# Kernel optimization log

Measured on AMD Instinct MI355X. Metric: run time of the kernel, lower is better.

## Reference

```python
import jax, jax.numpy as jnp
import numpy as np

K = 8            # hard-coded knn k
NS = 0.2         # LeakyReLU negative slope
EPS = 1e-6
LN_EPS = 1e-5
H = 6            # num_heads


def vn_lin(W, x):
    # VNLinear: linear over vector-channel dim (axis 1). x: (B, Cin, 3, ...)
    return jnp.einsum('oc,bc...->bo...', W, x)


def vn_leaky(x, W, U):
    # VNLinearLeakyReLU (no BN): feature map p, direction map d
    p = vn_lin(W, x)
    d = vn_lin(U, x)
    dot = jnp.sum(p * d, axis=2, keepdims=True)
    dsq = jnp.sum(d * d, axis=2, keepdims=True)
    neg = p - (dot / (dsq + EPS)) * d
    return NS * p + (1.0 - NS) * jnp.where(dot >= 0, p, neg)


def vn_layernorm(x, g, b):
    # LayerNorm on per-channel vector norms, rescale directions. x: (B,C,3,N)
    n = jnp.sqrt(jnp.sum(x * x, axis=2) + EPS)            # (B,C,N)
    mu = jnp.mean(n, axis=1, keepdims=True)
    var = jnp.var(n, axis=1, keepdims=True)
    nhat = (n - mu) / jnp.sqrt(var + LN_EPS)
    nnew = g[None, :, None] * nhat + b[None, :, None]
    return x * (nnew / n)[:, :, None, :]


def vn_attention(vn_x, Wq, Wk, Wv, Wo):
    # vn_x: (B, C, 3, N); VNLinear(C, 3C) projections, multi-head SDPA over N
    B, C, _, N = vn_x.shape
    def heads(W):
        t = vn_lin(W, vn_x)                               # (B, 3C, 3, N)
        t = t.reshape(B, H, 3 * C // H, 3, N)
        return t.transpose(0, 1, 4, 2, 3).reshape(B, H, N, -1)  # (B,H,N,9C/H)
    q, k, v = heads(Wq), heads(Wk), heads(Wv)
    scale = (3 * C // H) ** -0.5                          # head_dim = dim//H = 64
    attn = jax.nn.softmax(jnp.einsum('bhqd,bhkd->bhqk', q, k) * scale, axis=-1)
    o = jnp.einsum('bhqk,bhkd->bhqd', attn, v)            # (B,H,N,9C/H)
    o = o.transpose(0, 2, 1, 3).reshape(B, N, 3 * C, 3).transpose(0, 2, 3, 1)
    return vn_lin(Wo, o)                                  # (B, C, 3, N)


def vn_get_graph_feature(x, knn_index):
    # x: (B, C, 3, N); knn_index: flat (B*K*N,) into (B*N) rows
    B, C, _, N = x.shape
    xp = x.transpose(0, 3, 1, 2).reshape(B * N, C * 3)
    feat = xp[knn_index].reshape(B, K, N, C, 3)
    xc = x.transpose(0, 3, 1, 2).reshape(B, 1, N, C, 3)
    f = jnp.concatenate([feat - xc, jnp.broadcast_to(xc, (B, K, N, C, 3))], axis=3)
    return f.transpose(0, 3, 4, 2, 1)                     # (B, 2C, 3, N, K)


def setup_inputs() -> dict:
    key = jax.random.key(0)
    ks = jax.random.split(key, 20)
    B, N, C = 4, 2048, 128
    def w(k, o, i):
        return jax.random.normal(k, (o, i), jnp.float32) * (i ** -0.5)
    return {
        'x': jax.random.normal(ks[0], (B, N, 3 * C), jnp.float32),
        'knn_index': jax.random.randint(ks[1], (B * K * N,), 0, B * N),
        'g1': jnp.ones((C,), jnp.float32), 'b1': jnp.zeros((C,), jnp.float32),
        'g2': jnp.ones((C,), jnp.float32), 'b2': jnp.zeros((C,), jnp.float32),
        'Wq': w(ks[2], 3 * C, C), 'Wk': w(ks[3], 3 * C, C), 'Wv': w(ks[4], 3 * C, C),
        'Wo': w(ks[5], C, 3 * C),
        'W1': w(ks[6], C, 2 * C), 'U1': w(ks[7], C, 2 * C),   # conv1: 256->128
        'W2': w(ks[8], C, 2 * C),                               # conv2: 256->128
        'W3': w(ks[9], 2 * C, C), 'U3': w(ks[10], 2 * C, C),   # conv3: 128->256
        'W4': w(ks[11], C, 2 * C), 'U4': w(ks[12], C, 2 * C),  # conv4: 256->128
    }


def reference(x, knn_index, g1, b1, g2, b2, Wq, Wk, Wv, Wo, W1, U1, W2, W3, U3, W4, U4):
    B, N, D = x.shape
    C = D // 3
    vn_x = x.transpose(0, 2, 1).reshape(B, C, 3, N)
    norm_x = vn_layernorm(vn_x, g1, b1)
    x_1 = vn_attention(norm_x, Wq, Wk, Wv, Wo)            # (B,C,3,N)
    knn_f = vn_get_graph_feature(norm_x, knn_index)       # (B,2C,3,N,K)
    knn_f = vn_leaky(knn_f, W1, U1)                       # (B,C,3,N,K)
    knn_f = jnp.mean(knn_f, axis=-1)                      # mean_pool over k
    x_1 = jnp.concatenate([x_1, knn_f], axis=1)           # (B,2C,3,N)
    x_1 = vn_lin(W2, x_1)                                 # (B,C,3,N)
    vn_x = vn_x + x_1
    nx2 = vn_layernorm(vn_x, g2, b2)
    h = vn_leaky(nx2, W3, U3)                             # (B,2C,3,N)
    h = vn_leaky(h, W4, U4)                               # (B,C,3,N)
    vn_x = vn_x + h
    return vn_x.reshape(B, D, N).transpose(0, 2, 1)       # (B,N,384)
```

## Files before the change

kernel.cpp:

```cpp
#include <hip/hip_runtime.h>
#include <math.h>

#define NFIX 2048
#define HH 6
#define KNN 8
#define NSLOPE 0.2f
#define EPSF 1e-6f
#define LNEPSF 1e-5f
#define QSCALE 0.18033688011112042f
#define NSPLIT 2

typedef unsigned short ushort_t;
typedef unsigned int uint_t;
typedef __attribute__((ext_vector_type(8))) short bf16x8;
typedef __attribute__((ext_vector_type(4))) short bf16x4;
typedef __attribute__((ext_vector_type(8))) _Float16 f16x8;
typedef __attribute__((ext_vector_type(4))) _Float16 f16x4;
typedef __attribute__((ext_vector_type(16))) float f32x16;
typedef __attribute__((ext_vector_type(4))) float f32x4;

__device__ __forceinline__ ushort_t f2bf(float f) {
  union { float f; unsigned u; } v; v.f = f;
  unsigned r = v.u + 0x7fff + ((v.u >> 16) & 1);
  return (ushort_t)(r >> 16);
}
__device__ __forceinline__ float bf2f(ushort_t u) {
  union { uint_t u; float f; } v; v.u = ((uint_t)u) << 16; return v.f;
}
__device__ __forceinline__ uint_t pack2(float a, float b) {
  return (uint_t)f2bf(a) | ((uint_t)f2bf(b) << 16);
}
__device__ __forceinline__ ushort_t f2h_bits(float a) {
  union { _Float16 h; ushort_t s; } cv; cv.h = (_Float16)a; return cv.s;
}
__device__ __forceinline__ uint_t packh2(float a, float b) {
  union { _Float16 h; ushort_t s; } ha, hb;
  ha.h = (_Float16)a; hb.h = (_Float16)b;
  return (uint_t)ha.s | ((uint_t)hb.s << 16);
}

__device__ __forceinline__ void vnleaky3(const float* p, const float* dv, float* out) {
  float dot = p[0]*dv[0] + p[1]*dv[1] + p[2]*dv[2];
  float dsq = dv[0]*dv[0] + dv[1]*dv[1] + dv[2]*dv[2] + EPSF;
  float f = dot / dsq;
#pragma unroll
  for (int d = 0; d < 3; ++d) {
    float neg = p[d] - f * dv[d];
    out[d] = NSLOPE * p[d] + (1.f - NSLOPE) * ((dot >= 0.f) ? p[d] : neg);
  }
}

__global__ __launch_bounds__(256) void prep_ln1(
    const float* __restrict__ Wq, const float* __restrict__ Wk,
    const float* __restrict__ Wv, const float* __restrict__ Wo,
    const float* __restrict__ W1, const float* __restrict__ U1,
    const float* __restrict__ W2, const float* __restrict__ W3,
    const float* __restrict__ U3, const float* __restrict__ W4,
    const float* __restrict__ U4,
    ushort_t* __restrict__ Wall, _Float16* __restrict__ Af16,
    _Float16* __restrict__ W3h, _Float16* __restrict__ U3h,
    _Float16* __restrict__ W4h, _Float16* __restrict__ U4h,
    const float* __restrict__ xin, ushort_t* __restrict__ xbp,
    float* __restrict__ xdi, const float* __restrict__ g1,
    const float* __restrict__ b1) {
  __shared__ float red[8];
  int bi = blockIdx.x;
  if (bi >= 1600) {
    int t = threadIdx.x;
    int half = t >> 7, c = t & 127;
    int bn = (bi - 1600) * 2 + half;
    const float* row = xin + (size_t)bn * 384;
    float x0 = row[c*3+0], x1 = row[c*3+1], x2 = row[c*3+2];
    float nv = sqrtf(x0*x0 + x1*x1 + x2*x2 + EPSF);
    float s1 = nv, s2 = nv*nv;
#pragma unroll
    for (int off = 32; off >= 1; off >>= 1) {
      s1 += __shfl_down(s1, off);
      s2 += __shfl_down(s2, off);
    }
    int lane = t & 63, w = t >> 6;
    if (lane == 0) { red[w*2] = s1; red[w*2+1] = s2; }
    __syncthreads();
    int rb4 = (w >> 1) * 4;
    float tot1 = red[rb4] + red[rb4+2], tot2 = red[rb4+1] + red[rb4+3];
    float mu  = tot1 * (1.f/128.f);
    float var = tot2 * (1.f/128.f) - mu*mu;
    float rsig = rsqrtf(var + LNEPSF);
    float nnew = g1[c] * ((nv - mu) * rsig) + b1[c];
    float sc = nnew / nv;
    size_t rb = (size_t)bn * 384;
    xbp[rb + c]       = f2bf(x0*sc);
    xbp[rb + 128 + c] = f2bf(x1*sc);
    xbp[rb + 256 + c] = f2bf(x2*sc);
    xdi[rb + c]       = x0;
    xdi[rb + 128 + c] = x1;
    xdi[rb + 256 + c] = x2;
    return;
  }
  int idx = bi * 256 + threadIdx.x;
  if (idx < 212992) {
    int m = idx >> 7, c = idx & 127;
    float val;
    if (m < 384)       val = Wq[m*128 + c] * QSCALE;
    else if (m < 768)  val = Wk[(m-384)*128 + c];
    else if (m < 1152) val = Wv[(m-768)*128 + c];
    else {
      int j = m - 1152;
      if (j < 128)      val = W1[j*256 + c];
      else if (j < 256) val = U1[(j-128)*256 + c];
      else if (j < 384) { int o = j-256; val = W1[o*256 + 128 + c] - W1[o*256 + c]; }
      else              { int o = j-384; val = U1[o*256 + 128 + c] - U1[o*256 + c]; }
    }
    Wall[idx] = f2bf(val); return;
  }
  idx -= 212992;
  if (idx < 49152) {
    int c = idx / 384, j = idx % 384;
    float s = 0.f;
    for (int cp = 0; cp < 128; ++cp) s += W2[c*256 + cp] * Wo[cp*384 + j];
    Af16[(size_t)c*512 + j] = (_Float16)s; return;
  }
  idx -= 49152;
  if (idx < 16384) {
    int c2 = idx / 128, c = idx % 128;
    Af16[(size_t)c*512 + 384 + c2] = (_Float16)W2[c*256 + 128 + c2]; return;
  }
  idx -= 16384;
  if (idx < 32768) { W3h[idx] = (_Float16)W3[idx]; return; }
  idx -= 32768;
  if (idx < 32768) { U3h[idx] = (_Float16)U3[idx]; return; }
  idx -= 32768;
  if (idx < 32768) { W4h[idx] = (_Float16)W4[idx]; return; }
  idx -= 32768;
  if (idx < 32768) { U4h[idx] = (_Float16)U4[idx]; return; }
}

#define XT_PITCH 132
#define WT_PITCH 132
#define TR_PITCH 36
__global__ __launch_bounds__(256, 2) void qkv_conv1_mfma(
    const ushort_t* __restrict__ xb, const ushort_t* __restrict__ Wall,
    ushort_t* __restrict__ q, ushort_t* __restrict__ k, ushort_t* __restrict__ v,
    _Float16* __restrict__ YZh, _Float16* __restrict__ NBh) {
  __shared__ ushort_t xs[128*XT_PITCH];
  __shared__ ushort_t wt[2][32*WT_PITCH];
  __shared__ float tr[4][32*TR_PITCH];
  int nb = blockIdx.x % 192;
  int mq = blockIdx.x / 192;
  int n0 = nb * 128;
  int t = threadIdx.x;
  int w = t >> 6, lane = t & 63, ql = lane & 31, hl = lane >> 5;
  for (int idx = t; idx < 2048; idx += 256) {
    int n = idx >> 4, c16 = idx & 15;
    bf16x8 gv = *(const bf16x8*)&xb[(size_t)(n0 + n)*128 + c16*8];
    ushort_t* dst = &xs[n*XT_PITCH + c16*8];
    *(bf16x4*)dst = __builtin_shufflevector(gv, gv, 0, 1, 2, 3);
    *(bf16x4*)(dst+4) = __builtin_shufflevector(gv, gv, 4, 5, 6, 7);
  }
#pragma unroll
  for (int i = 0; i < 2; ++i) {
    int idx = i*256 + t;
    int mm = idx >> 4, c16 = idx & 15;
    bf16x8 gv = *(const bf16x8*)&Wall[(size_t)(mq*416 + mm)*128 + c16*8];
    ushort_t* dst = &wt[0][mm*WT_PITCH + c16*8];
    *(bf16x4*)dst = __builtin_shufflevector(gv, gv, 0, 1, 2, 3);
    *(bf16x4*)(dst+4) = __builtin_shufflevector(gv, gv, 4, 5, 6, 7);
  }
  __syncthreads();
  bf16x8 xf[8];
  {
    const ushort_t* xr = &xs[(w*32 + ql)*XT_PITCH + hl*8];
#pragma unroll
    for (int cs = 0; cs < 8; ++cs) {
      bf16x4 lo = *(const bf16x4*)(xr + cs*16);
      bf16x4 hi = *(const bf16x4*)(xr + cs*16 + 4);
      xf[cs] = __builtin_shufflevector(lo, hi, 0, 1, 2, 3, 4, 5, 6, 7);
    }
  }
  int ng = n0 + w*32 + ql;
  int pt = ng / 3;
  int d  = ng - 3*pt;
  float* trw = tr[w];
  int mm0 = t >> 4, c160 = t & 15;
  int mm1 = (t + 256) >> 4, c161 = t & 15;
  for (int mt = 0; mt < 13; ++mt) {
    int m0 = mq*416 + mt*32;
    int cur = mt & 1;
    bf16x8 wpre0, wpre1;
    if (mt < 12) {
      int m0n = m0 + 32;
      wpre0 = *(const bf16x8*)&Wall[(size_t)(m0n + mm0)*128 + c160*8];
      wpre1 = *(const bf16x8*)&Wall[(size_t)(m0n + mm1)*128 + c161*8];
    }
    f32x16 acc;
#pragma unroll
    for (int r = 0; r < 16; ++r) acc[r] = 0.f;
    const ushort_t* wr = &wt[cur][ql*WT_PITCH + hl*8];
#pragma unroll
    for (int cs = 0; cs < 8; ++cs) {
      bf16x4 lo = *(const bf16x4*)(wr + cs*16);
      bf16x4 hi = *(const bf16x4*)(wr + cs*16 + 4);
      bf16x8 af = __builtin_shufflevector(lo, hi, 0, 1, 2, 3, 4, 5, 6, 7);
      acc = __builtin_amdgcn_mfma_f32_32x32x16_bf16(af, xf[cs], acc, 0, 0, 0);
    }
#pragma unroll
    for (int r = 0; r < 16; ++r) {
      int mrow = (r&3) + 8*(r>>2) + 4*hl;
      trw[ql*TR_PITCH + mrow] = acc[r];
    }
    asm volatile("s_waitcnt lgkmcnt(0)" ::: "memory");
    float4 c0 = *(float4*)&trw[ql*TR_PITCH + hl*16 + 0];
    float4 c1 = *(float4*)&trw[ql*TR_PITCH + hl*16 + 4];
    float4 c2 = *(float4*)&trw[ql*TR_PITCH + hl*16 + 8];
    float4 c3 = *(float4*)&trw[ql*TR_PITCH + hl*16 + 12];
    asm volatile("s_waitcnt lgkmcnt(0)" ::: "memory");
    int mg = m0 + hl*16;
    if (m0 < 1152) {
      uint4 s0, s1;
      s0.x = pack2(c0.x, c0.y); s0.y = pack2(c0.z, c0.w);
      s0.z = pack2(c1.x, c1.y); s0.w = pack2(c1.z, c1.w);
      s1.x = pack2(c2.x, c2.y); s1.y = pack2(c2.z, c2.w);
      s1.z = pack2(c3.x, c3.y); s1.w = pack2(c3.z, c3.w);
      ushort_t* dst;
      if (m0 < 384)       dst = q + (size_t)pt*1152 + d*384 + mg;
      else if (m0 < 768)  dst = k + (size_t)pt*1152 + d*384 + (mg - 384);
      else                dst = v + (size_t)pt*1152 + d*384 + (mg - 768);
      *(uint4*)dst = s0;
      *(uint4*)(dst + 8) = s1;
    } else {
      int mat = mg - 1152;
      int sub = mat >> 7, o = mat & 127;
      _Float16* basep = (sub < 2) ? YZh : NBh;
      _Float16* dst = basep + (size_t)pt*768 + d*256 + (sub & 1)*128 + o;
      uint4 s0, s1;
      s0.x = packh2(c0.x, c0.y); s0.y = packh2(c0.z, c0.w);
      s0.z = packh2(c1.x, c1.y); s0.w = packh2(c1.z, c1.w);
      s1.x = packh2(c2.x, c2.y); s1.y = packh2(c2.z, c2.w);
      s1.z = packh2(c3.x, c3.y); s1.w = packh2(c3.z, c3.w);
      *(uint4*)dst = s0;
      *(uint4*)(dst + 8) = s1;
    }
    if (mt < 12) {
      int nxt = cur ^ 1;
      ushort_t* d0 = &wt[nxt][mm0*WT_PITCH + c160*8];
      *(bf16x4*)d0 = __builtin_shufflevector(wpre0, wpre0, 0, 1, 2, 3);
      *(bf16x4*)(d0+4) = __builtin_shufflevector(wpre0, wpre0, 4, 5, 6, 7);
      ushort_t* d1 = &wt[nxt][mm1*WT_PITCH + c161*8];
      *(bf16x4*)d1 = __builtin_shufflevector(wpre1, wpre1, 0, 1, 2, 3);
      *(bf16x4*)(d1+4) = __builtin_shufflevector(wpre1, wpre1, 4, 5, 6, 7);
    }
    __syncthreads();
  }
}

#define VT_LP 196
__global__ __launch_bounds__(256) void post_vtrans(const ushort_t* __restrict__ v,
    ushort_t* __restrict__ vT, const _Float16* __restrict__ YZh,
    const _Float16* __restrict__ NBh, const int* __restrict__ knn_index,
    _Float16* __restrict__ kmf16) {
  __shared__ ushort_t tl[64*VT_LP];
  __shared__ int sidx[8][KNN];
  int blk = blockIdx.x;
  int t = threadIdx.x;
  if (blk < 768) {
    int bh = blk / 32, ptile = blk % 32;
    int b = bh / HH, h = bh % HH;
    int pt0 = ptile * 64;
#pragma unroll
    for (int i = 0; i < 6; ++i) {
      int u = i*256 + t;
      int p = u / 24, seg = u % 24;
      int d = seg >> 3, c8 = seg & 7;
      bf16x8 gv = *(const bf16x8*)&v[(size_t)(b*NFIX + pt0 + p)*1152 + d*384 + h*64 + c8*8];
      ushort_t* dst = &tl[p*VT_LP + d*64 + c8*8];
      *(bf16x4*)dst = __builtin_shufflevector(gv, gv, 0, 1, 2, 3);
      *(bf16x4*)(dst+4) = __builtin_shufflevector(gv, gv, 4, 5, 6, 7);
    }
    __syncthreads();
#pragma unroll
    for (int i = 0; i < 6; ++i) {
      int u = i*256 + t;
      int ch = u >> 3, pc = u & 7;
      int ol = ch / 3, dd = ch - 3*ol;
      int cloc = dd*64 + ol;
      ushort_t hv[8];
#pragma unroll
      for (int e = 0; e < 8; ++e)
        hv[e] = tl[(pc*8 + e)*VT_LP + cloc];
      uint4 o4;
      o4.x = (uint_t)hv[0] | ((uint_t)hv[1] << 16);
      o4.y = (uint_t)hv[2] | ((uint_t)hv[3] << 16);
      o4.z = (uint_t)hv[4] | ((uint_t)hv[5] << 16);
      o4.w = (uint_t)hv[6] | ((uint_t)hv[7] << 16);
      *(uint4*)&vT[((size_t)bh*192 + ch)*2048 + pt0 + pc*8] = o4;
    }
    return;
  }
  int bnb = (blk - 768) * 8;
  int half = t >> 7, c = t & 127;
  if (t < 64) {
    int pi = t >> 3, kk = t & 7;
    int bn = bnb + pi;
    int b = bn / NFIX, n = bn % NFIX;
    sidx[pi][kk] = knn_index[(b*KNN + kk)*NFIX + n];
  }
  __syncthreads();
#pragma unroll
  for (int pi2 = 0; pi2 < 4; ++pi2) {
    int pi = half*4 + pi2;
    int bn = bnb + pi;
    float yb[3], zb[3];
#pragma unroll
    for (int d = 0; d < 3; ++d) {
      yb[d] = (float)NBh[(size_t)bn*768 + d*256 + c];
      zb[d] = (float)NBh[(size_t)bn*768 + d*256 + 128 + c];
    }
    float om[3] = {0.f, 0.f, 0.f};
#pragma unroll
    for (int kk = 0; kk < KNN; ++kk) {
      const _Float16* r = YZh + (size_t)sidx[pi][kk]*768;
      float p[3], dd[3];
#pragma unroll
      for (int d = 0; d < 3; ++d) {
        p[d]  = (float)r[d*256 + c] + yb[d];
        dd[d] = (float)r[d*256 + 128 + c] + zb[d];
      }
      float res[3];
      vnleaky3(p, dd, res);
      om[0] += res[0]; om[1] += res[1]; om[2] += res[2];
    }
#pragma unroll
    for (int d = 0; d < 3; ++d)
      kmf16[((size_t)bn*3 + d)*128 + c] = (_Float16)(om[d] * (1.f/KNN));
  }
}

#define KT_P 196
#define VT_P 36
#define TW_P 195
__global__ __launch_bounds__(256, 2) void attn_kernel(const ushort_t* __restrict__ q,
    const ushort_t* __restrict__ k, const ushort_t* __restrict__ vT,
    ushort_t* __restrict__ opart, float* __restrict__ lpart) {
  __shared__ ushort_t kt[2][32*KT_P];
  __shared__ ushort_t vt[2][192*VT_P];
  __shared__ float alds[4][32];
  int blk = blockIdx.x;
  int xcd = blk & 7, j = blk >> 3;
  int g = xcd*6 + (j >> 4);
  int qt = j & 15;
  int bh = g % 24;
  int split = g / 24;
  int b = bh / HH, h = bh % HH;
  int t = threadIdx.x;
  int w = t >> 6, lane = t & 63, ql = lane & 31, hl = lane >> 5;
  int qrow0 = qt*128 + w*32;
  const ushort_t* qpb = q + (size_t)(b*NFIX + qrow0 + ql)*1152 + h*64;
  bf16x8 qf[12];
#pragma unroll
  for (int cs = 0; cs < 12; ++cs) {
    int red0 = cs*16 + hl*8;
    int dq = red0 >> 6, ml = red0 & 63;
    qf[cs] = *(const bf16x8*)(qpb + dq*384 + ml);
  }
  const ushort_t* ksrc[3]; int kdsto[3];
  const ushort_t* vsrc[3]; int vdsto[3];
#pragma unroll
  for (int j2 = 0; j2 < 3; ++j2) {
    int idx = t + j2*256;
    int kp = idx / 24, c16 = idx % 24;
    int red0 = c16*8;
    int dk = red0 >> 6, ml = red0 & 63;
    ksrc[j2] = k + (size_t)(b*NFIX + kp)*1152 + dk*384 + h*64 + ml;
    kdsto[j2] = kp*KT_P + c16*8;
    int ch = idx >> 2, c4 = idx & 3;
    vsrc[j2] = vT + ((size_t)bh*192 + ch)*2048 + c4*8;
    vdsto[j2] = ch*VT_P + c4*8;
  }
  f32x16 acc[6];
#pragma unroll
  for (int nt = 0; nt < 6; ++nt)
#pragma unroll
    for (int r = 0; r < 16; ++r) acc[nt][r] = 0.f;
  float lsum = 0.f;
  int koff0 = split * 1024;
  bf16x8 kpre[3], vpre[3];
#pragma unroll
  for (int j2 = 0; j2 < 3; ++j2) {
    kpre[j2] = *(const bf16x8*)(ksrc[j2] + (size_t)koff0*1152);
    vpre[j2] = *(const bf16x8*)(vsrc[j2] + koff0);
  }
#pragma unroll
  for (int j2 = 0; j2 < 3; ++j2) {
    ushort_t* kd = &kt[0][kdsto[j2]];
    *(bf16x4*)kd = __builtin_shufflevector(kpre[j2], kpre[j2], 0, 1, 2, 3);
    *(bf16x4*)(kd+4) = __builtin_shufflevector(kpre[j2], kpre[j2], 4, 5, 6, 7);
    ushort_t* vd = &vt[0][vdsto[j2]];
    *(bf16x4*)vd = __builtin_shufflevector(vpre[j2], vpre[j2], 0, 1, 2, 3);
    *(bf16x4*)(vd+4) = __builtin_shufflevector(vpre[j2], vpre[j2], 4, 5, 6, 7);
  }
  __syncthreads();
  for (int kb = 0; kb < 32; ++kb) {
    int cur = kb & 1;
    if (kb < 31) {
      int koff = koff0 + (kb+1)*32;
#pragma unroll
      for (int j2 = 0; j2 < 3; ++j2) {
        kpre[j2] = *(const bf16x8*)(ksrc[j2] + (size_t)koff*1152);
        vpre[j2] = *(const bf16x8*)(vsrc[j2] + koff);
      }
    }
    f32x16 sca, scb;
#pragma unroll
    for (int r = 0; r < 16; ++r) { sca[r] = 0.f; scb[r] = 0.f; }
    const ushort_t* ktc = kt[cur];
#pragma unroll
    for (int cs = 0; cs < 12; ++cs) {
      const ushort_t* kr = &ktc[ql*KT_P + cs*16 + hl*8];
      bf16x4 alo = *(const bf16x4*)kr;
      bf16x4 ahi = *(const bf16x4*)(kr + 4);
      bf16x8 af = __builtin_shufflevector(alo, ahi, 0, 1, 2, 3, 4, 5, 6, 7);
      if (cs & 1) scb = __builtin_amdgcn_mfma_f32_32x32x16_bf16(af, qf[cs], scb, 0, 0, 0);
      else        sca = __builtin_amdgcn_mfma_f32_32x32x16_bf16(af, qf[cs], sca, 0, 0, 0);
    }
    uint_t u[8], pex[8];
#pragma unroll
    for (int g2 = 0; g2 < 4; ++g2) {
      float p0 = __builtin_amdgcn_exp2f(sca[g2*4 + 0] + scb[g2*4 + 0]);
      float p1 = __builtin_amdgcn_exp2f(sca[g2*4 + 1] + scb[g2*4 + 1]);
      float p2 = __builtin_amdgcn_exp2f(sca[g2*4 + 2] + scb[g2*4 + 2]);
      float p3 = __builtin_amdgcn_exp2f(sca[g2*4 + 3] + scb[g2*4 + 3]);
      lsum += (p0 + p1) + (p2 + p3);
      u[2*g2]   = pack2(p0, p1);
      u[2*g2+1] = pack2(p2, p3);
    }
#pragma unroll
    for (int j2 = 0; j2 < 8; ++j2) pex[j2] = (uint_t)__shfl_xor((int)u[j2], 32);
    const ushort_t* vtc = vt[cur];
#pragma unroll
    for (int s = 0; s < 2; ++s) {
      uint4 au;
      au.x = hl ? pex[4*s+2] : u[4*s+0];
      au.y = hl ? pex[4*s+3] : u[4*s+1];
      au.z = hl ? u[4*s+2]   : pex[4*s+0];
      au.w = hl ? u[4*s+3]   : pex[4*s+1];
      union { uint4 ui; bf16x8 bv; } cvt; cvt.ui = au;
      bf16x8 pa = cvt.bv;
#pragma unroll
      for (int nt = 0; nt < 6; ++nt) {
        const ushort_t* vr = &vtc[(nt*32 + ql)*VT_P + s*16 + hl*8];
        bf16x4 vlo = *(const bf16x4*)vr;
        bf16x4 vhi = *(const bf16x4*)(vr + 4);
        bf16x8 vf = __builtin_shufflevector(vlo, vhi, 0, 1, 2, 3, 4, 5, 6, 7);
        acc[nt] = __builtin_amdgcn_mfma_f32_32x32x16_bf16(pa, vf, acc[nt], 0, 0, 0);
      }
    }
    if (kb < 31) {
      int nxt = cur ^ 1;
#pragma unroll
      for (int j2 = 0; j2 < 3; ++j2) {
        ushort_t* kd = &kt[nxt][kdsto[j2]];
        *(bf16x4*)kd = __builtin_shufflevector(kpre[j2], kpre[j2], 0, 1, 2, 3);
        *(bf16x4*)(kd+4) = __builtin_shufflevector(kpre[j2], kpre[j2], 4, 5, 6, 7);
        ushort_t* vd = &vt[nxt][vdsto[j2]];
        *(bf16x4*)vd = __builtin_shufflevector(vpre[j2], vpre[j2], 0, 1, 2, 3);
        *(bf16x4*)(vd+4) = __builtin_shufflevector(vpre[j2], vpre[j2], 4, 5, 6, 7);
      }
    }
    __syncthreads();
  }
  lsum += __shfl_xor(lsum, 32);
  if (lane < 32) {
    alds[w][ql] = 1.0f / lsum;
    lpart[(size_t)split*24*NFIX + (size_t)bh*NFIX + qrow0 + ql] = lsum;
  }
  asm volatile("s_waitcnt lgkmcnt(0)" ::: "memory");
  float lv[4][4];
#pragma unroll
  for (int g2 = 0; g2 < 4; ++g2) {
    f32x4 tv = *(const f32x4*)&alds[w][8*g2 + 4*hl];
#pragma unroll
    for (int rr = 0; rr < 4; ++rr) lv[g2][rr] = tv[rr];
  }
  ushort_t* tw = (w == 0) ? kt[0] : (w == 1) ? kt[1] : (w == 2) ? vt[0] : vt[1];
#pragma unroll
  for (int nt = 0; nt < 6; ++nt) {
    int ch = nt*32 + ql;
#pragma unroll
    for (int r = 0; r < 16; ++r) {
      int qrow = (r&3) + 8*(r>>2) + 4*hl;
      tw[qrow*TW_P + ch] = f2h_bits(acc[nt][r] * lv[r>>2][r&3]);
    }
  }
  asm volatile("s_waitcnt lgkmcnt(0)" ::: "memory");
  const size_t SS = (size_t)8192*1152;
  ushort_t* opb = opart + (size_t)split*SS;
  size_t nbase = (size_t)(b*NFIX + qrow0) * 3;
#pragma unroll
  for (int i = 0; i < 12; ++i) {
    int chunk = i*64 + lane;
    int nl = chunk >> 3, jc = chunk & 7;
    int qq = nl / 3, dd = nl - 3*qq;
    ushort_t hv[8];
#pragma unroll
    for (int e = 0; e < 8; ++e)
      hv[e] = tw[qq*TW_P + (jc*8 + e)*3 + dd];
    uint4 sv;
    sv.x = (uint_t)hv[0] | ((uint_t)hv[1] << 16);
    sv.y = (uint_t)hv[2] | ((uint_t)hv[3] << 16);
    sv.z = (uint_t)hv[4] | ((uint_t)hv[5] << 16);
    sv.w = (uint_t)hv[6] | ((uint_t)hv[7] << 16);
    *(uint4*)&opb[(nbase + nl)*384 + h*64 + jc*8] = sv;
  }
}

#define AP 68
#define XLP 132
__global__ __launch_bounds__(768) void x1mid_mfma(
    const float* __restrict__ xdi, const ushort_t* __restrict__ opart,
    const float* __restrict__ lpart, const _Float16* __restrict__ kmf16,
    const _Float16* __restrict__ Af16, float* __restrict__ xmid,
    _Float16* __restrict__ nxh, const float* __restrict__ g2,
    const float* __restrict__ b2) {
  __shared__ __align__(16) char smem[50944];
  _Float16* As = (_Float16*)smem;
  _Float16* Bt = (_Float16*)(smem + 17408);
  float* wlsL  = (float*)(smem + 30464);
  float* X     = (float*)smem;
  float* stats = (float*)(smem + 50688);
  int blk = blockIdx.x;
  int n0 = blk * 96;
  int pt0 = blk * 32;
  int t = threadIdx.x;
  int w = t >> 6, lane = t & 63, ql = lane & 31, hl = lane >> 5;
  int nsub = w >> 2, mt2 = w & 3;
  if (t < 192) {
    int ptl = t / 6, h = t % 6;
    int ptg = pt0 + ptl;
    int b = ptg >> 11, n = ptg & 2047;
    size_t lidx = (size_t)(b*HH + h)*NFIX + n;
    float l[NSPLIT]; float tot = 0.f;
#pragma unroll
    for (int s = 0; s < NSPLIT; ++s) {
      l[s] = lpart[(size_t)s*24*NFIX + lidx];
      tot += l[s];
    }
    float rd = 1.f / tot;
    float* wp = &wlsL[(ptl*6 + h)*NSPLIT];
#pragma unroll
    for (int s = 0; s < NSPLIT; ++s) wp[s] = l[s]*rd;
  }
  f32x16 acc;
#pragma unroll
  for (int r = 0; r < 16; ++r) acc[r] = 0.f;
  const size_t SS = (size_t)8192*1152;
  __syncthreads();
  for (int p = 0; p < 8; ++p) {
    for (int u = t; u < 1024; u += 768) {
      int m = u >> 3, kc = u & 7;
      f16x4 a0 = *(const f16x4*)&Af16[(size_t)m*512 + p*64 + kc*8];
      f16x4 a1 = *(const f16x4*)&Af16[(size_t)m*512 + p*64 + kc*8 + 4];
      _Float16* dst = &As[m*AP + kc*8];
      *(f16x4*)dst = a0;
      *(f16x4*)(dst+4) = a1;
    }
    {
      int n_l = t >> 3, jc = t & 7;
      int n_g = n0 + n_l;
      _Float16* dst = &Bt[n_l*AP + jc*8];
      if (p < 6) {
        int pt_l = n_l / 3;
        const float* wp = &wlsL[(pt_l*6 + p)*NSPLIT];
        float facc[8];
#pragma unroll
        for (int e = 0; e < 8; ++e) facc[e] = 0.f;
#pragma unroll
        for (int s = 0; s < NSPLIT; ++s) {
          const ushort_t* src = opart + s*SS + (size_t)n_g*384 + p*64 + jc*8;
          uint4 ra = *(const uint4*)src;
          const _Float16* ua = (const _Float16*)&ra;
          float wsc = wp[s];
#pragma unroll
          for (int e = 0; e < 8; ++e)
            facc[e] += wsc * (float)ua[e];
        }
        _Float16 hv[8];
#pragma unroll
        for (int e = 0; e < 8; ++e) hv[e] = (_Float16)facc[e];
        *(f16x4*)dst = *(f16x4*)&hv[0];
        *(f16x4*)(dst+4) = *(f16x4*)&hv[4];
      } else {
        const _Float16* src = kmf16 + (size_t)n_g*128 + (p-6)*64 + jc*8;
        f16x4 v0 = *(const f16x4*)src;
        f16x4 v1 = *(const f16x4*)(src + 4);
        *(f16x4*)dst = v0; *(f16x4*)(dst+4) = v1;
      }
    }
    __syncthreads();
#pragma unroll
    for (int cs = 0; cs < 4; ++cs) {
      int kloc = cs*16 + hl*8;
      f16x4 b0 = *(const f16x4*)&Bt[(nsub*32 + ql)*AP + kloc];
      f16x4 b1 = *(const f16x4*)&Bt[(nsub*32 + ql)*AP + kloc + 4];
      f16x8 bf = __builtin_shufflevector(b0, b1, 0, 1, 2, 3, 4, 5, 6, 7);
      int mrow = mt2*32 + ql;
      f16x4 a0 = *(const f16x4*)&As[mrow*AP + kloc];
      f16x4 a1 = *(const f16x4*)&As[mrow*AP + kloc + 4];
      f16x8 af = __builtin_shufflevector(a0, a1, 0, 1, 2, 3, 4, 5, 6, 7);
      acc = __builtin_amdgcn_mfma_f32_32x32x16_f16(af, bf, acc, 0, 0, 0);
    }
    __syncthreads();
  }
  {
    int cbase = mt2*32 + 4*hl;
    float* xrow = &X[(nsub*32 + ql)*XLP];
#pragma unroll
    for (int r = 0; r < 16; ++r) {
      int col = cbase + (r&3) + 8*(r>>2);
      xrow[col] = acc[r];
    }
  }
  __syncthreads();
#pragma unroll
  for (int i = 0; i < 2; ++i) {
    int u = i*768 + t;
    int row = u >> 4, c0 = (u & 15) * 8;
    float* xp = &X[row*XLP + c0];
    const float* xd = xdi + (size_t)(n0 + row)*128 + c0;
    float4 a0 = *(float4*)xp, a1 = *(float4*)(xp + 4);
    float4 d0 = *(const float4*)xd, d1 = *(const float4*)(xd + 4);
    a0.x += d0.x; a0.y += d0.y; a0.z += d0.z; a0.w += d0.w;
    a1.x += d1.x; a1.y += d1.y; a1.z += d1.z; a1.w += d1.w;
    *(float4*)xp = a0; *(float4*)(xp + 4) = a1;
    float* dst = xmid + (size_t)(n0 + row)*128 + c0;
    *(float4*)dst = a0; *(float4*)(dst + 4) = a1;
  }
  __syncthreads();
  for (int pi = w; pi < 32; pi += 12) {
    int c = lane;
    float a0 = X[(pi*3+0)*XLP + c], a1 = X[(pi*3+1)*XLP + c], a2 = X[(pi*3+2)*XLP + c];
    float e0 = X[(pi*3+0)*XLP + c + 64], e1 = X[(pi*3+1)*XLP + c + 64], e2 = X[(pi*3+2)*XLP + c + 64];
    float nva = sqrtf(a0*a0 + a1*a1 + a2*a2 + EPSF);
    float nvb = sqrtf(e0*e0 + e1*e1 + e2*e2 + EPSF);
    float s1 = nva + nvb;
    float s2 = nva*nva + nvb*nvb;
#pragma unroll
    for (int off = 32; off >= 1; off >>= 1) {
      s1 += __shfl_down(s1, off);
      s2 += __shfl_down(s2, off);
    }
    if (lane == 0) {
      float mu = s1 * (1.f/128.f);
      float var = s2 * (1.f/128.f) - mu*mu;
      stats[pi*2]   = mu;
      stats[pi*2+1] = rsqrtf(var + LNEPSF);
    }
  }
  __syncthreads();
#pragma unroll
  for (int i = 0; i < 2; ++i) {
    int u = i*768 + t;
    int row = u >> 4, c0 = (u & 15) * 8;
    int pt_l = row / 3;
    float mu = stats[pt_l*2], rsig = stats[pt_l*2+1];
    const float* r0 = &X[(pt_l*3 + 0)*XLP + c0];
    const float* r1 = &X[(pt_l*3 + 1)*XLP + c0];
    const float* r2 = &X[(pt_l*3 + 2)*XLP + c0];
    const float* rd = &X[row*XLP + c0];
    float xv[8];
#pragma unroll
    for (int e = 0; e < 8; ++e) {
      float x0 = r0[e], x1 = r1[e], x2 = r2[e];
      float nv = sqrtf(x0*x0 + x1*x1 + x2*x2 + EPSF);
      float nnew = g2[c0 + e] * ((nv - mu) * rsig) + b2[c0 + e];
      xv[e] = rd[e] * (nnew / nv);
    }
    uint4 sv;
    sv.x = packh2(xv[0], xv[1]); sv.y = packh2(xv[2], xv[3]);
    sv.z = packh2(xv[4], xv[5]); sv.w = packh2(xv[6], xv[7]);
    *(uint4*)&nxh[(size_t)(n0 + row)*128 + c0] = sv;
  }
}

#define X3P 132
#define HP4 260
#define TF4P 388
__global__ __launch_bounds__(512) void conv34_fused(const _Float16* __restrict__ nxh,
    const _Float16* __restrict__ W3h, const _Float16* __restrict__ U3h,
    const _Float16* __restrict__ W4h, const _Float16* __restrict__ U4h,
    const float* __restrict__ xmid, float* __restrict__ out) {
  __shared__ __align__(16) char smem[49920];
  _Float16* Xs3 = (_Float16*)smem;
  _Float16* H   = (_Float16*)smem;
  float* trF    = (float*)smem;
  int pt0 = blockIdx.x * 32;
  int t = threadIdx.x;
  int w = t >> 6, lane = t & 63, ql = lane & 31, hl = lane >> 5;
#pragma unroll
  for (int i = 0; i < 3; ++i) {
    int u = i*512 + t;
    int r = u >> 4, c8 = u & 15;
    f16x8 gv = *(const f16x8*)&nxh[(size_t)(pt0*3 + r)*128 + c8*8];
    int d = r % 3, p = r / 3;
    _Float16* dst = &Xs3[(d*32 + p)*X3P + c8*8];
    *(f16x4*)dst = __builtin_shufflevector(gv, gv, 0, 1, 2, 3);
    *(f16x4*)(dst+4) = __builtin_shufflevector(gv, gv, 4, 5, 6, 7);
  }
  __syncthreads();
  int ot3 = w*32;
  const _Float16* Wp = W3h + (size_t)(ot3 + ql)*128 + hl*8;
  const _Float16* Up = U3h + (size_t)(ot3 + ql)*128 + hl*8;
  f32x16 accP[3], accD[3];
#pragma unroll
  for (int d = 0; d < 3; ++d)
#pragma unroll
    for (int r = 0; r < 16; ++r) { accP[d][r] = 0.f; accD[d][r] = 0.f; }
#pragma unroll
  for (int cs = 0; cs < 8; ++cs) {
    f16x8 wf = *(const f16x8*)(Wp + cs*16);
    f16x8 uf = *(const f16x8*)(Up + cs*16);
#pragma unroll
    for (int d = 0; d < 3; ++d) {
      const _Float16* xr = &Xs3[(d*32 + ql)*X3P + cs*16 + hl*8];
      f16x4 lo = *(const f16x4*)xr;
      f16x4 hi = *(const f16x4*)(xr + 4);
      f16x8 xf = __builtin_shufflevector(lo, hi, 0, 1, 2, 3, 4, 5, 6, 7);
      accP[d] = __builtin_amdgcn_mfma_f32_32x32x16_f16(wf, xf, accP[d], 0, 0, 0);
      accD[d] = __builtin_amdgcn_mfma_f32_32x32x16_f16(uf, xf, accD[d], 0, 0, 0);
    }
  }
  __syncthreads();
#pragma unroll
  for (int r = 0; r < 16; ++r) {
    int olr = (r&3) + 8*(r>>2) + 4*hl;
    float p3[3], d3[3], res[3];
#pragma unroll
    for (int d = 0; d < 3; ++d) { p3[d] = accP[d][r]; d3[d] = accD[d][r]; }
    vnleaky3(p3, d3, res);
#pragma unroll
    for (int d = 0; d < 3; ++d)
      H[(d*32 + ql)*HP4 + ot3 + olr] = (_Float16)res[d];
  }
  __syncthreads();
  int ph = w >> 2;
  int ot4 = (w & 3) * 32;
  int nl = lane & 15, kq = lane >> 4;
  f32x4 acc4P[2][3], acc4D[2][3];
#pragma unroll
  for (int mt = 0; mt < 2; ++mt)
#pragma unroll
    for (int d = 0; d < 3; ++d)
#pragma unroll
      for (int r = 0; r < 4; ++r) { acc4P[mt][d][r] = 0.f; acc4D[mt][d][r] = 0.f; }
  const _Float16* Wb = W4h + (size_t)ot4*256;
  const _Float16* Ub = U4h + (size_t)ot4*256;
#pragma unroll
  for (int cs = 0; cs < 8; ++cs) {
    int kof = cs*32 + kq*8;
    f16x8 xf[3];
#pragma unroll
    for (int d = 0; d < 3; ++d) {
      const _Float16* xr = &H[(d*32 + ph*16 + nl)*HP4 + kof];
      f16x4 lo = *(const f16x4*)xr;
      f16x4 hi = *(const f16x4*)(xr + 4);
      xf[d] = __builtin_shufflevector(lo, hi, 0, 1, 2, 3, 4, 5, 6, 7);
    }
#pragma unroll
    for (int mt = 0; mt < 2; ++mt) {
      f16x8 wf = *(const f16x8*)(Wb + (size_t)(mt*16 + nl)*256 + kof);
      f16x8 uf = *(const f16x8*)(Ub + (size_t)(mt*16 + nl)*256 + kof);
#pragma unroll
      for (int d = 0; d < 3; ++d) {
        acc4P[mt][d] = __builtin_amdgcn_mfma_f32_16x16x32_f16(wf, xf[d], acc4P[mt][d], 0, 0, 0);
        acc4D[mt][d] = __builtin_amdgcn_mfma_f32_16x16x32_f16(uf, xf[d], acc4D[mt][d], 0, 0, 0);
      }
    }
  }
  __syncthreads();
#pragma unroll
  for (int mt = 0; mt < 2; ++mt)
#pragma unroll
    for (int r = 0; r < 4; ++r) {
      int o = ot4 + mt*16 + kq*4 + r;
      int p_l = ph*16 + nl;
      float p3[3], d3[3], res[3];
#pragma unroll
      for (int d = 0; d < 3; ++d) { p3[d] = acc4P[mt][d][r]; d3[d] = acc4D[mt][d][r]; }
      vnleaky3(p3, d3, res);
#pragma unroll
      for (int d = 0; d < 3; ++d) trF[p_l*TF4P + o*3 + d] = res[d];
    }
  __syncthreads();
#pragma unroll
  for (int i = 0; i < 6; ++i) {
    int u = i*512 + t;
    int row = u / 96, c4 = u % 96;
    float4 vv = *(float4*)&trF[row*TF4P + c4*4];
    int bn = pt0 + row;
    float rs[4];
    const float* fv = (const float*)&vv;
#pragma unroll
    for (int e = 0; e < 4; ++e) {
      int col = c4*4 + e;
      int o = col / 3, d = col - 3*o;
      rs[e] = fv[e] + xmid[(size_t)(3*bn + d)*128 + o];
    }
    float4 ov; ov.x = rs[0]; ov.y = rs[1]; ov.z = rs[2]; ov.w = rs[3];
    *(float4*)&out[(size_t)bn*384 + c4*4] = ov;
  }
}

extern "C" void kernel_launch(void* const* d_in, const int* in_sizes, int n_in,
                              void* d_out, int out_size, void* d_ws, size_t ws_size,
                              hipStream_t stream) {
  const float* x   = (const float*)d_in[0];
  const int* knn   = (const int*)d_in[1];
  const float* g1  = (const float*)d_in[2];
  const float* b1  = (const float*)d_in[3];
  const float* g2  = (const float*)d_in[4];
  const float* b2  = (const float*)d_in[5];
  const float* Wq  = (const float*)d_in[6];
  const float* Wk  = (const float*)d_in[7];
  const float* Wv  = (const float*)d_in[8];
  const float* Wo  = (const float*)d_in[9];
  const float* W1  = (const float*)d_in[10];
  const float* U1  = (const float*)d_in[11];
  const float* W2  = (const float*)d_in[12];
  const float* W3  = (const float*)d_in[13];
  const float* U3  = (const float*)d_in[14];
  const float* W4  = (const float*)d_in[15];
  const float* U4  = (const float*)d_in[16];
  float* out = (float*)d_out;
  (void)n_in; (void)out_size; (void)ws_size;

  const size_t BN = (size_t)in_sizes[0] / 384;

  float* ws    = (float*)d_ws;
  float* xdi   = ws;
  float* xmid  = xdi + BN*384;
  _Float16* kmf16 = (_Float16*)(xmid + BN*384);
  ushort_t* xbp = (ushort_t*)(kmf16 + BN*384);
  ushort_t* qb = xbp + BN*384;
  ushort_t* kb = qb + BN*1152;
  ushort_t* vb = kb + BN*1152;
  ushort_t* vT = vb + BN*1152;
  ushort_t* Wall = vT + BN*1152;
  _Float16* Af16 = (_Float16*)(Wall + 212992);
  _Float16* W3h = Af16 + 65536;
  _Float16* U3h = W3h + 32768;
  _Float16* W4h = U3h + 32768;
  _Float16* U4h = W4h + 32768;
  ushort_t* opart = (ushort_t*)(U4h + 32768);
  float* lpart = (float*)(opart + 4*BN*1152);
  _Float16* YZh = (_Float16*)opart;
  _Float16* NBh = YZh + BN*768;
  _Float16* nxh = (_Float16*)qb;

  prep_ln1<<<1600 + 4096, 256, 0, stream>>>(Wq, Wk, Wv, Wo, W1, U1, W2, W3, U3, W4, U4,
                                            Wall, Af16, W3h, U3h, W4h, U4h,
                                            x, xbp, xdi, g1, b1);
  qkv_conv1_mfma<<<192*4, 256, 0, stream>>>(xbp, Wall, qb, kb, vb, YZh, NBh);
  post_vtrans<<<768 + 1024, 256, 0, stream>>>(vb, vT, YZh, NBh, knn, kmf16);
  attn_kernel<<<16*24*NSPLIT, 256, 0, stream>>>(qb, kb, vT, opart, lpart);
  x1mid_mfma<<<256, 768, 0, stream>>>(xdi, opart, lpart, kmf16, Af16, xmid, nxh, g2, b2);
  conv34_fused<<<256, 512, 0, stream>>>(nxh, W3h, U3h, W4h, U4h, xmid, out);
}
```

Baseline: 298.5 us.

## Fuse x1mid and conv3/conv4 kernels into one block-level kernel

Merges the x1mid kernel and conv34_fused into a single 768-thread kernel. The residual xmid values are held in registers and the normalized nx tile is written straight into shared memory, so the global round trip for xmid and nxh and one launch are removed. Four of the twelve waves sit idle during the conv3/conv4 MFMA phases. Each thread also keeps 16 extra floats live across the whole kernel, which adds register pressure.

New measurement: 294.6 us. No clear change (-1.3%).

```diff
diff --git a/kernel.cpp b/kernel.cpp
--- a/kernel.cpp
+++ b/kernel.cpp
@@ -515,18 +515,26 @@
 
 #define AP 68
 #define XLP 132
-__global__ __launch_bounds__(768) void x1mid_mfma(
+#define X3P 132
+#define HP4 260
+#define TF4P 388
+__global__ __launch_bounds__(768) void x1mid_c34(
     const float* __restrict__ xdi, const ushort_t* __restrict__ opart,
     const float* __restrict__ lpart, const _Float16* __restrict__ kmf16,
-    const _Float16* __restrict__ Af16, float* __restrict__ xmid,
-    _Float16* __restrict__ nxh, const float* __restrict__ g2,
-    const float* __restrict__ b2) {
+    const _Float16* __restrict__ Af16, const float* __restrict__ g2,
+    const float* __restrict__ b2,
+    const _Float16* __restrict__ W3h, const _Float16* __restrict__ U3h,
+    const _Float16* __restrict__ W4h, const _Float16* __restrict__ U4h,
+    float* __restrict__ out) {
   __shared__ __align__(16) char smem[50944];
   _Float16* As = (_Float16*)smem;
   _Float16* Bt = (_Float16*)(smem + 17408);
   float* wlsL  = (float*)(smem + 30464);
   float* X     = (float*)smem;
   float* stats = (float*)(smem + 50688);
+  _Float16* Xs3 = (_Float16*)smem;
+  _Float16* H   = (_Float16*)smem;
+  float* trF    = (float*)smem;
   int blk = blockIdx.x;
   int n0 = blk * 96;
   int pt0 = blk * 32;
@@ -631,10 +639,20 @@
     a0.x += d0.x; a0.y += d0.y; a0.z += d0.z; a0.w += d0.w;
     a1.x += d1.x; a1.y += d1.y; a1.z += d1.z; a1.w += d1.w;
     *(float4*)xp = a0; *(float4*)(xp + 4) = a1;
-    float* dst = xmid + (size_t)(n0 + row)*128 + c0;
-    *(float4*)dst = a0; *(float4*)(dst + 4) = a1;
-  }
-  __syncthreads();
+  }
+  __syncthreads();
+  float rs[16];
+#pragma unroll
+  for (int i = 0; i < 4; ++i) {
+    int u = i*768 + t;
+    int row = u / 96, c4 = u % 96;
+#pragma unroll
+    for (int e = 0; e < 4; ++e) {
+      int col = c4*4 + e;
+      int o = col / 3, dd = col - 3*o;
+      rs[i*4 + e] = X[(3*row + dd)*XLP + o];
+    }
+  }
   for (int pi = w; pi < 32; pi += 12) {
     int c = lane;
     float a0 = X[(pi*3+0)*XLP + c], a1 = X[(pi*3+1)*XLP + c], a2 = X[(pi*3+2)*XLP + c];
@@ -656,6 +674,7 @@
     }
   }
   __syncthreads();
+  uint4 svr[2]; int rowr[2], c0r[2];
 #pragma unroll
   for (int i = 0; i < 2; ++i) {
     int u = i*768 + t;
@@ -677,134 +696,123 @@
     uint4 sv;
     sv.x = packh2(xv[0], xv[1]); sv.y = packh2(xv[2], xv[3]);
     sv.z = packh2(xv[4], xv[5]); sv.w = packh2(xv[6], xv[7]);
-    *(uint4*)&nxh[(size_t)(n0 + row)*128 + c0] = sv;
-  }
-}
-
-#define X3P 132
-#define HP4 260
-#define TF4P 388
-__global__ __launch_bounds__(512) void conv34_fused(const _Float16* __restrict__ nxh,
-    const _Float16* __restrict__ W3h, const _Float16* __restrict__ U3h,
-    const _Float16* __restrict__ W4h, const _Float16* __restrict__ U4h,
-    const float* __restrict__ xmid, float* __restrict__ out) {
-  __shared__ __align__(16) char smem[49920];
-  _Float16* Xs3 = (_Float16*)smem;
-  _Float16* H   = (_Float16*)smem;
-  float* trF    = (float*)smem;
-  int pt0 = blockIdx.x * 32;
-  int t = threadIdx.x;
-  int w = t >> 6, lane = t & 63, ql = lane & 31, hl = lane >> 5;
-#pragma unroll
-  for (int i = 0; i < 3; ++i) {
-    int u = i*512 + t;
-    int r = u >> 4, c8 = u & 15;
-    f16x8 gv = *(const f16x8*)&nxh[(size_t)(pt0*3 + r)*128 + c8*8];
-    int d = r % 3, p = r / 3;
-    _Float16* dst = &Xs3[(d*32 + p)*X3P + c8*8];
-    *(f16x4*)dst = __builtin_shufflevector(gv, gv, 0, 1, 2, 3);
-    *(f16x4*)(dst+4) = __builtin_shufflevector(gv, gv, 4, 5, 6, 7);
-  }
-  __syncthreads();
+    svr[i] = sv; rowr[i] = row; c0r[i] = c0;
+  }
+  __syncthreads();
+#pragma unroll
+  for (int i = 0; i < 2; ++i) {
+    int row = rowr[i];
+    int d = row % 3, p = row / 3;
+    _Float16* dst = &Xs3[(d*32 + p)*X3P + c0r[i]];
+    uint2 lo; lo.x = svr[i].x; lo.y = svr[i].y;
+    uint2 hi; hi.x = svr[i].z; hi.y = svr[i].w;
+    *(uint2*)dst = lo;
+    *(uint2*)(dst + 4) = hi;
+  }
+  __syncthreads();
+  f32x16 accP[3], accD[3];
   int ot3 = w*32;
-  const _Float16* Wp = W3h + (size_t)(ot3 + ql)*128 + hl*8;
-  const _Float16* Up = U3h + (size_t)(ot3 + ql)*128 + hl*8;
-  f32x16 accP[3], accD[3];
-#pragma unroll
-  for (int d = 0; d < 3; ++d)
-#pragma unroll
-    for (int r = 0; r < 16; ++r) { accP[d][r] = 0.f; accD[d][r] = 0.f; }
-#pragma unroll
-  for (int cs = 0; cs < 8; ++cs) {
-    f16x8 wf = *(const f16x8*)(Wp + cs*16);
-    f16x8 uf = *(const f16x8*)(Up + cs*16);
-#pragma unroll
-    for (int d = 0; d < 3; ++d) {
-      const _Float16* xr = &Xs3[(d*32 + ql)*X3P + cs*16 + hl*8];
-      f16x4 lo = *(const f16x4*)xr;
-      f16x4 hi = *(const f16x4*)(xr + 4);
-      f16x8 xf = __builtin_shufflevector(lo, hi, 0, 1, 2, 3, 4, 5, 6, 7);
-      accP[d] = __builtin_amdgcn_mfma_f32_32x32x16_f16(wf, xf, accP[d], 0, 0, 0);
-      accD[d] = __builtin_amdgcn_mfma_f32_32x32x16_f16(uf, xf, accD[d], 0, 0, 0);
-    }
-  }
-  __syncthreads();
-#pragma unroll
-  for (int r = 0; r < 16; ++r) {
-    int olr = (r&3) + 8*(r>>2) + 4*hl;
-    float p3[3], d3[3], res[3];
-#pragma unroll
-    for (int d = 0; d < 3; ++d) { p3[d] = accP[d][r]; d3[d] = accD[d][r]; }
-    vnleaky3(p3, d3, res);
+  if (w < 8) {
 #pragma unroll
     for (int d = 0; d < 3; ++d)
-      H[(d*32 + ql)*HP4 + ot3 + olr] = (_Float16)res[d];
+#pragma unroll
+      for (int r = 0; r < 16; ++r) { accP[d][r] = 0.f; accD[d][r] = 0.f; }
+    const _Float16* Wp = W3h + (size_t)(ot3 + ql)*128 + hl*8;
+    const _Float16* Up = U3h + (size_t)(ot3 + ql)*128 + hl*8;
+#pragma unroll
+    for (int cs = 0; cs < 8; ++cs) {
+      f16x8 wf = *(const f16x8*)(Wp + cs*16);
+      f16x8 uf = *(const f16x8*)(Up + cs*16);
+#pragma unroll
+      for (int d = 0; d < 3; ++d) {
+        const _Float16* xr = &Xs3[(d*32 + ql)*X3P + cs*16 + hl*8];
+        f16x4 lo = *(const f16x4*)xr;
+        f16x4 hi = *(const f16x4*)(xr + 4);
+        f16x8 xf = __builtin_shufflevector(lo, hi, 0, 1, 2, 3, 4, 5, 6, 7);
+        accP[d] = __builtin_amdgcn_mfma_f32_32x32x16_f16(wf, xf, accP[d], 0, 0, 0);
+        accD[d] = __builtin_amdgcn_mfma_f32_32x32x16_f16(uf, xf, accD[d], 0, 0, 0);
+      }
+    }
+  }
+  __syncthreads();
+  if (w < 8) {
+#pragma unroll
+    for (int r = 0; r < 16; ++r) {
+      int olr = (r&3) + 8*(r>>2) + 4*hl;
+      float p3[3], d3[3], res[3];
+#pragma unroll
+      for (int d = 0; d < 3; ++d) { p3[d] = accP[d][r]; d3[d] = accD[d][r]; }
+      vnleaky3(p3, d3, res);
+#pragma unroll
+      for (int d = 0; d < 3; ++d)
+        H[(d*32 + ql)*HP4 + ot3 + olr] = (_Float16)res[d];
+    }
   }
   __syncthreads();
   int ph = w >> 2;
   int ot4 = (w & 3) * 32;
   int nl = lane & 15, kq = lane >> 4;
   f32x4 acc4P[2][3], acc4D[2][3];
-#pragma unroll
-  for (int mt = 0; mt < 2; ++mt)
-#pragma unroll
-    for (int d = 0; d < 3; ++d)
-#pragma unroll
-      for (int r = 0; r < 4; ++r) { acc4P[mt][d][r] = 0.f; acc4D[mt][d][r] = 0.f; }
-  const _Float16* Wb = W4h + (size_t)ot4*256;
-  const _Float16* Ub = U4h + (size_t)ot4*256;
-#pragma unroll
-  for (int cs = 0; cs < 8; ++cs) {
-    int kof = cs*32 + kq*8;
-    f16x8 xf[3];
-#pragma unroll
-    for (int d = 0; d < 3; ++d) {
-      const _Float16* xr = &H[(d*32 + ph*16 + nl)*HP4 + kof];
-      f16x4 lo = *(const f16x4*)xr;
-      f16x4 hi = *(const f16x4*)(xr + 4);
-      xf[d] = __builtin_shufflevector(lo, hi, 0, 1, 2, 3, 4, 5, 6, 7);
-    }
-#pragma unroll
-    for (int mt = 0; mt < 2; ++mt) {
-      f16x8 wf = *(const f16x8*)(Wb + (size_t)(mt*16 + nl)*256 + kof);
-      f16x8 uf = *(const f16x8*)(Ub + (size_t)(mt*16 + nl)*256 + kof);
+  if (w < 8) {
+#pragma unroll
+    for (int mt = 0; mt < 2; ++mt)
+#pragma unroll
+      for (int d = 0; d < 3; ++d)
+#pragma unroll
+        for (int r = 0; r < 4; ++r) { acc4P[mt][d][r] = 0.f; acc4D[mt][d][r] = 0.f; }
+    const _Float16* Wb = W4h + (size_t)ot4*256;
+    const _Float16* Ub = U4h + (size_t)ot4*256;
+#pragma unroll
+    for (int cs = 0; cs < 8; ++cs) {
+      int kof = cs*32 + kq*8;
+      f16x8 xf[3];
 #pragma unroll
       for (int d = 0; d < 3; ++d) {
-        acc4P[mt][d] = __builtin_amdgcn_mfma_f32_16x16x32_f16(wf, xf[d], acc4P[mt][d], 0, 0, 0);
-        acc4D[mt][d] = __builtin_amdgcn_mfma_f32_16x16x32_f16(uf, xf[d], acc4D[mt][d], 0, 0, 0);
+        const _Float16* xr = &H[(d*32 + ph*16 + nl)*HP4 + kof];
+        f16x4 lo = *(const f16x4*)xr;
+        f16x4 hi = *(const f16x4*)(xr + 4);
+        xf[d] = __builtin_shufflevector(lo, hi, 0, 1, 2, 3, 4, 5, 6, 7);
       }
-    }
-  }
-  __syncthreads();
-#pragma unroll
-  for (int mt = 0; mt < 2; ++mt)
-#pragma unroll
-    for (int r = 0; r < 4; ++r) {
-      int o = ot4 + mt*16 + kq*4 + r;
-      int p_l = ph*16 + nl;
-      float p3[3], d3[3], res[3];
-#pragma unroll
-      for (int d = 0; d < 3; ++d) { p3[d] = acc4P[mt][d][r]; d3[d] = acc4D[mt][d][r]; }
-      vnleaky3(p3, d3, res);
-#pragma unroll
-      for (int d = 0; d < 3; ++d) trF[p_l*TF4P + o*3 + d] = res[d];
-    }
-  __syncthreads();
-#pragma unroll
-  for (int i = 0; i < 6; ++i) {
-    int u = i*512 + t;
+#pragma unroll
+      for (int mt = 0; mt < 2; ++mt) {
+        f16x8 wf = *(const f16x8*)(Wb + (size_t)(mt*16 + nl)*256 + kof);
+        f16x8 uf = *(const f16x8*)(Ub + (size_t)(mt*16 + nl)*256 + kof);
+#pragma unroll
+        for (int d = 0; d < 3; ++d) {
+          acc4P[mt][d] = __builtin_amdgcn_mfma_f32_16x16x32_f16(wf, xf[d], acc4P[mt][d], 0, 0, 0);
+          acc4D[mt][d] = __builtin_amdgcn_mfma_f32_16x16x32_f16(uf, xf[d], acc4D[mt][d], 0, 0, 0);
+        }
+      }
+    }
+  }
+  __syncthreads();
+  if (w < 8) {
+#pragma unroll
+    for (int mt = 0; mt < 2; ++mt)
+#pragma unroll
+      for (int r = 0; r < 4; ++r) {
+        int o = ot4 + mt*16 + kq*4 + r;
+        int p_l = ph*16 + nl;
+        float p3[3], d3[3], res[3];
+#pragma unroll
+        for (int d = 0; d < 3; ++d) { p3[d] = acc4P[mt][d][r]; d3[d] = acc4D[mt][d][r]; }
+        vnleaky3(p3, d3, res);
+#pragma unroll
+        for (int d = 0; d < 3; ++d) trF[p_l*TF4P + o*3 + d] = res[d];
+      }
+  }
+  __syncthreads();
+#pragma unroll
+  for (int i = 0; i < 4; ++i) {
+    int u = i*768 + t;
     int row = u / 96, c4 = u % 96;
     float4 vv = *(float4*)&trF[row*TF4P + c4*4];
     int bn = pt0 + row;
-    float rs[4];
-    const float* fv = (const float*)&vv;
-#pragma unroll
-    for (int e = 0; e < 4; ++e) {
-      int col = c4*4 + e;
-      int o = col / 3, d = col - 3*o;
-      rs[e] = fv[e] + xmid[(size_t)(3*bn + d)*128 + o];
-    }
-    float4 ov; ov.x = rs[0]; ov.y = rs[1]; ov.z = rs[2]; ov.w = rs[3];
+    float4 ov;
+    ov.x = vv.x + rs[i*4 + 0];
+    ov.y = vv.y + rs[i*4 + 1];
+    ov.z = vv.z + rs[i*4 + 2];
+    ov.w = vv.w + rs[i*4 + 3];
     *(float4*)&out[(size_t)bn*384 + c4*4] = ov;
   }
 }
@@ -853,7 +861,6 @@
   float* lpart = (float*)(opart + 4*BN*1152);
   _Float16* YZh = (_Float16*)opart;
   _Float16* NBh = YZh + BN*768;
-  _Float16* nxh = (_Float16*)qb;
 
   prep_ln1<<<1600 + 4096, 256, 0, stream>>>(Wq, Wk, Wv, Wo, W1, U1, W2, W3, U3, W4, U4,
                                             Wall, Af16, W3h, U3h, W4h, U4h,
@@ -861,6 +868,6 @@
   qkv_conv1_mfma<<<192*4, 256, 0, stream>>>(xbp, Wall, qb, kb, vb, YZh, NBh);
   post_vtrans<<<768 + 1024, 256, 0, stream>>>(vb, vT, YZh, NBh, knn, kmf16);
   attn_kernel<<<16*24*NSPLIT, 256, 0, stream>>>(qb, kb, vT, opart, lpart);
-  x1mid_mfma<<<256, 768, 0, stream>>>(xdi, opart, lpart, kmf16, Af16, xmid, nxh, g2, b2);
-  conv34_fused<<<256, 512, 0, stream>>>(nxh, W3h, U3h, W4h, U4h, xmid, out);
-}
+  x1mid_c34<<<256, 768, 0, stream>>>(xdi, opart, lpart, kmf16, Af16, g2, b2,
+                                     W3h, U3h, W4h, U4h, out);
+}
```
